# Kernel optimization log

Measured on AMD Instinct MI355X. Metric: run time of the kernel, lower is better.

Reference implementation:

```python
import jax, jax.numpy as jnp
import numpy as np

EPS = 1e-10
REG_WEIGHT = 1e-6  # regularization_weight passed to sparse_image_warp


def _phi(r):
    # TPS order-2 kernel on SQUARED distances r: 0.5 * r * log(r)
    return 0.5 * r * jnp.log(jnp.maximum(r, EPS))


def _sq_dist(a, b):
    # a: [b, n, 2], b: [b, m, 2] -> [b, n, m] squared euclidean distances
    aa = jnp.sum(a * a, axis=-1)[:, :, None]
    bb = jnp.sum(b * b, axis=-1)[:, None, :]
    ab = jnp.einsum('bnd,bmd->bnm', a, b)
    return jnp.maximum(aa + bb - 2.0 * ab, 0.0)


def interpolate_spline(train_points, train_values, query_points, reg_weight):
    # Solve polyharmonic (TPS, order 2) interpolation and evaluate at query points.
    b, n, _ = train_points.shape
    dt = train_points.dtype
    A = _phi(_sq_dist(train_points, train_points)) + reg_weight * jnp.eye(n, dtype=dt)
    B = jnp.concatenate([train_points, jnp.ones((b, n, 1), dt)], axis=-1)  # [b, n, 3]
    k = B.shape[-1]
    lhs = jnp.concatenate([
        jnp.concatenate([A, B], axis=-1),
        jnp.concatenate([jnp.swapaxes(B, 1, 2), jnp.zeros((b, k, k), dt)], axis=-1),
    ], axis=1)                                                             # [b, n+3, n+3]
    rhs = jnp.concatenate([train_values, jnp.zeros((b, k, train_values.shape[-1]), dt)], axis=1)
    sol = jnp.linalg.solve(lhs, rhs)
    w, v = sol[:, :n], sol[:, n:]                                          # [b,n,2], [b,3,2]
    Q = _phi(_sq_dist(query_points, train_points))                         # [b, m, n]
    qb = jnp.concatenate([query_points, jnp.ones((*query_points.shape[:2], 1), dt)], axis=-1)
    return Q @ w + qb @ v                                                  # [b, m, 2]


def dense_image_warp(image, flow):
    # image: [b, c, h, w] (NCHW), flow: [b, h, w, 2] in (y, x); sample at grid - flow.
    b, c, h, w = image.shape
    gy, gx = jnp.meshgrid(jnp.arange(h, dtype=flow.dtype),
                          jnp.arange(w, dtype=flow.dtype), indexing='ij')
    qy = jnp.clip(gy[None] - flow[..., 0], 0.0, h - 1.0)                  # [b, h, w]
    qx = jnp.clip(gx[None] - flow[..., 1], 0.0, w - 1.0)
    y0 = jnp.clip(jnp.floor(qy).astype(jnp.int32), 0, h - 2)
    x0 = jnp.clip(jnp.floor(qx).astype(jnp.int32), 0, w - 2)
    y1, x1 = y0 + 1, x0 + 1
    wy = (qy - y0.astype(flow.dtype))[..., None]                          # [b, h, w, 1]
    wx = (qx - x0.astype(flow.dtype))[..., None]
    bidx = jnp.arange(b)[:, None, None]

    def gather(yi, xi):
        # -> [b, h, w, c]
        return image[bidx, :, yi, xi]

    top = gather(y0, x0) * (1.0 - wx) + gather(y0, x1) * wx
    bot = gather(y1, x0) * (1.0 - wx) + gather(y1, x1) * wx
    out = top * (1.0 - wy) + bot * wy                                     # [b, h, w, c]
    return jnp.transpose(out, (0, 3, 1, 2))                               # back to NCHW


def sparse_image_warp(image, src_pts, dst_pts, reg_weight):
    # flows at control points, interpolated to a dense flow, then resample.
    b, _, h, w = image.shape
    flows = dst_pts - src_pts                                              # [b, n, 2]
    gy, gx = jnp.meshgrid(jnp.arange(h, dtype=src_pts.dtype),
                          jnp.arange(w, dtype=src_pts.dtype), indexing='ij')
    grid = jnp.stack([gy, gx], axis=-1).reshape(1, h * w, 2)
    query = jnp.broadcast_to(grid, (b, h * w, 2))
    dense_flow = interpolate_spline(dst_pts, flows, query, reg_weight).reshape(b, h, w, 2)
    return dense_image_warp(image, dense_flow), dense_flow


def setup_inputs() -> dict:
    key = jax.random.key(0)
    ks = jax.random.split(key, 10)
    B, C, H, W = 8, 3, 256, 256
    N_LDMARK = 68
    in_features = C * H * W

    def kaiming(k, fan_out, fan_in):
        bound = np.sqrt(6.0 / fan_in)
        return jax.random.uniform(k, (fan_out, fan_in), jnp.float32, -bound, bound)

    landmarks_mean = (jax.random.normal(ks[3], (N_LDMARK, 2), jnp.float32) * 50.0
                      + jnp.array([0.5 * H, 0.5 * W], jnp.float32)).reshape(-1)
    return {
        'x': jax.random.normal(ks[0], (B, C, H, W), jnp.float32),
        'images_rendered': jax.random.normal(ks[1], (B, 64, H, W), jnp.float32),
        'scales': jax.random.uniform(ks[2], (B, 1), jnp.float32),
        'landmarks_mean': landmarks_mean,
        'W1': kaiming(ks[4], 128, in_features),
        'b1': jnp.zeros((128,), jnp.float32),
        'W2': kaiming(ks[5], N_LDMARK * 2, 128),
        'b2': jnp.zeros((N_LDMARK * 2,), jnp.float32),
        'W3': kaiming(ks[6], N_LDMARK * 2, 128),
        'b3': jnp.zeros((N_LDMARK * 2,), jnp.float32),
    }


def reference(x, images_rendered, scales, landmarks_mean, W1, b1, W2, b2, W3, b3):
    b = x.shape[0]
    n_ldmark = W2.shape[0] // 2
    h = x.reshape(b, -1) @ W1.T + b1                                       # [b, 128]
    landmarks_pred = h @ W2.T + b2 + landmarks_mean                        # [b, 2n]
    landmarks_disp = (h @ W3.T + b3) * scales.reshape(-1, 1)               # [b, 2n]
    src = jax.lax.stop_gradient(landmarks_pred).reshape(b, n_ldmark, 2)
    dst = jax.lax.stop_gradient(landmarks_pred + landmarks_disp).reshape(b, n_ldmark, 2)
    landmarks_norm = jnp.mean(jnp.sqrt(jnp.sum(jnp.square(src - dst), axis=(1, 2))))
    warped, _ = sparse_image_warp(images_rendered, src, dst, REG_WEIGHT)
    return warped, landmarks_pred, landmarks_norm
```

## Files before the change

kernel.cpp:

```cpp
#include <hip/hip_runtime.h>
#include <math.h>

#define NB    8
#define CIMG  64
#define HH    256
#define WW    256
#define NL    68
#define NP    136
#define JD    128
#define NSYS  71
#define NCOL  73
#define MPAD  75
#define NCHK  32
#define CHUNK4 1536
#define ROW4  49152

#define OUT_PRED 33554432
#define OUT_NORM 33555520

#define WS_PART 0
#define WS_NORM 32768
#define WS_DST  32784
#define WS_WV   33920

__global__ __launch_bounds__(256) void k1_gemv(const float* __restrict__ x,
                                               const float* __restrict__ W1,
                                               float* __restrict__ part) {
  const int jg  = blockIdx.x;
  const int ch  = blockIdx.y;
  const int tid = threadIdx.x;
  const float4* __restrict__ xv = (const float4*)x;
  const float4* __restrict__ wv = (const float4*)W1;

  float acc[4][8];
#pragma unroll
  for (int a = 0; a < 4; ++a)
#pragma unroll
    for (int b = 0; b < 8; ++b) acc[a][b] = 0.f;

  const int base = ch * CHUNK4;
#pragma unroll
  for (int it = 0; it < 6; ++it) {
    const int k4 = base + it * 256 + tid;
    float4 w[4];
#pragma unroll
    for (int jj = 0; jj < 4; ++jj)
      w[jj] = wv[(size_t)(jg * 4 + jj) * ROW4 + k4];
#pragma unroll
    for (int b = 0; b < 8; ++b) {
      const float4 xr = xv[(size_t)b * ROW4 + k4];
#pragma unroll
      for (int jj = 0; jj < 4; ++jj) {
        acc[jj][b] = fmaf(w[jj].x, xr.x, acc[jj][b]);
        acc[jj][b] = fmaf(w[jj].y, xr.y, acc[jj][b]);
        acc[jj][b] = fmaf(w[jj].z, xr.z, acc[jj][b]);
        acc[jj][b] = fmaf(w[jj].w, xr.w, acc[jj][b]);
      }
    }
  }
#pragma unroll
  for (int jj = 0; jj < 4; ++jj)
#pragma unroll
    for (int b = 0; b < 8; ++b) {
      float v = acc[jj][b];
      for (int o = 32; o > 0; o >>= 1) v += __shfl_down(v, o, 64);
      acc[jj][b] = v;
    }
  __shared__ float sred[4][32];
  const int lane = tid & 63, wid = tid >> 6;
  if (lane == 0) {
#pragma unroll
    for (int jj = 0; jj < 4; ++jj)
#pragma unroll
      for (int b = 0; b < 8; ++b) sred[wid][jj * 8 + b] = acc[jj][b];
  }
  __syncthreads();
  if (tid < 32) {
    const float s = sred[0][tid] + sred[1][tid] + sred[2][tid] + sred[3][tid];
    const int jj = tid >> 3, b = tid & 7;
    part[((size_t)ch * JD + jg * 4 + jj) * 8 + b] = s;
  }
}

__device__ __forceinline__ double sys_entry(int r, int c,
                                            const float* s_dst,
                                            const float* s_disp) {
  if (r < NL) {
    if (c < NL) {
      const double dy = (double)s_dst[2 * r]     - (double)s_dst[2 * c];
      const double dx = (double)s_dst[2 * r + 1] - (double)s_dst[2 * c + 1];
      const double d2 = dy * dy + dx * dx;
      double v = 0.5 * d2 * log(fmax(d2, 1e-10));
      if (r == c) v += 1e-6;
      return v;
    }
    if (c == 68) return (double)s_dst[2 * r];
    if (c == 69) return (double)s_dst[2 * r + 1];
    if (c == 70) return 1.0;
    return (double)s_disp[2 * r + (c - 71)];
  }
  if (c < NL) {
    const int q = r - NL;
    return (q == 0) ? (double)s_dst[2 * c] : (q == 1) ? (double)s_dst[2 * c + 1] : 1.0;
  }
  return 0.0;
}

__global__ __launch_bounds__(256) void k2_land_solve(
    const float* __restrict__ part, const float* __restrict__ scales,
    const float* __restrict__ lmean, const float* __restrict__ b1,
    const float* __restrict__ W2, const float* __restrict__ b2,
    const float* __restrict__ W3, const float* __restrict__ b3,
    float* __restrict__ out, float* __restrict__ ws) {
  const int b = blockIdx.x, tid = threadIdx.x;
  const int lane = tid & 63, wv = tid >> 6;
  __shared__ float  s_h[JD];
  __shared__ float  s_dst[NP];
  __shared__ float  s_disp[NP];
  __shared__ double M[NSYS][MPAD];
  __shared__ int    s_perm[NSYS];
  __shared__ double s_inv;
  __shared__ int    s_pivv;

  if (tid < JD) {
    float s = b1[tid];
#pragma unroll 8
    for (int c = 0; c < NCHK; ++c) s += part[((size_t)c * JD + tid) * 8 + b];
    s_h[tid] = s;
  }
  __syncthreads();

  const float scale_b = scales[b];
  if (tid < NP) {
    const float4* w2 = (const float4*)(W2 + (size_t)tid * JD);
    const float4* w3 = (const float4*)(W3 + (size_t)tid * JD);
    float a2 = 0.f, a3 = 0.f;
#pragma unroll 8
    for (int k = 0; k < 32; ++k) {
      const float4 u = w2[k], v = w3[k];
      const float h0 = s_h[4 * k], h1 = s_h[4 * k + 1];
      const float h2 = s_h[4 * k + 2], h3 = s_h[4 * k + 3];
      a2 = fmaf(u.x, h0, fmaf(u.y, h1, fmaf(u.z, h2, fmaf(u.w, h3, a2))));
      a3 = fmaf(v.x, h0, fmaf(v.y, h1, fmaf(v.z, h2, fmaf(v.w, h3, a3))));
    }
    const float pred = a2 + b2[tid] + lmean[tid];
    const float disp = (a3 + b3[tid]) * scale_b;
    out[OUT_PRED + b * NP + tid] = pred;
    s_dst[tid]  = pred + disp;
    s_disp[tid] = disp;
  }
  __syncthreads();

  if (tid < 64) {
    float s = 0.f;
    for (int i = tid; i < NP; i += 64) { const float d = s_disp[i]; s = fmaf(d, d, s); }
    for (int o = 32; o > 0; o >>= 1) s += __shfl_down(s, o, 64);
    if (tid == 0) ws[WS_NORM + b] = s;
  }
  if (tid < NP) ws[WS_DST + b * NP + tid] = s_dst[tid];

  for (int e = tid; e < NSYS * NCOL; e += 256) {
    const int r = e / NCOL, c = e - r * NCOL;
    M[r][c] = sys_entry(r, c, s_dst, s_disp);
  }
  __syncthreads();

  const int rowA = lane, rowB = lane + 64;
  const bool hasB = (rowB < NSYS);
  bool actA = true, actB = hasB;
  int slotA = 0, slotB = 0;

#pragma unroll 1
  for (int p = 0; p < NSYS; ++p) {
    if (wv == 0) {
      unsigned ua = actA ? ((__float_as_uint((float)fabs(M[rowA][p])) & 0xFFFFFF80u) | (unsigned)rowA) : 0u;
      unsigned ub = (actB) ? ((__float_as_uint((float)fabs(M[rowB][p])) & 0xFFFFFF80u) | (unsigned)rowB) : 0u;
      unsigned u = ua > ub ? ua : ub;
#pragma unroll
      for (int o = 1; o < 64; o <<= 1) {
        const unsigned v = __shfl_xor(u, o);
        if (v > u) u = v;
      }
      const int piv = (int)(u & 0x7Fu);
      if (lane == 0) {
        s_pivv = piv;
        s_perm[p] = piv;
        s_inv = 1.0 / M[piv][p];
      }
    }
    __syncthreads();
    const int    piv = s_pivv;
    const double inv = s_inv;
    if (piv == rowA) { actA = false; slotA = p; }
    if (actB && piv == rowB) { actB = false; slotB = p; }
    const double mA = actA ? M[rowA][p] * inv : 0.0;
    const double mB = actB ? M[rowB][p] * inv : 0.0;

#pragma unroll 4
    for (int k = 0; k < 19; ++k) {
      const int c = wv + 4 * k;
      if (c > p && c < NCOL) {
        const double pvc = M[piv][c];
        if (actA) M[rowA][c] = fma(-mA, pvc, M[rowA][c]);
        if (actB) M[rowB][c] = fma(-mB, pvc, M[rowB][c]);
      }
    }
    __syncthreads();
  }

  if (wv == 0) {
    const int rpA = s_perm[lane];
    const int rpB = hasB ? s_perm[rowB] : 0;
    const double bb0a = M[rpA][NSYS], bb1a = M[rpA][NSYS + 1];
    const double diA = 1.0 / M[rpA][lane];
    double bb0b = 0.0, bb1b = 0.0, diB = 0.0;
    if (hasB) { bb0b = M[rpB][NSYS]; bb1b = M[rpB][NSYS + 1]; diB = 1.0 / M[rpB][rowB]; }
    double acc0a = 0.0, acc1a = 0.0, acc0b = 0.0, acc1b = 0.0;
    double sol0a = 0.0, sol1a = 0.0, sol0b = 0.0, sol1b = 0.0;
#pragma unroll 1
    for (int p = NSYS - 1; p >= 0; --p) {
      const double tA0 = (bb0a - acc0a) * diA;
      const double tA1 = (bb1a - acc1a) * diA;
      const double tB0 = (bb0b - acc0b) * diB;
      const double tB1 = (bb1b - acc1b) * diB;
      const bool fromB = (p >= 64);
      const int  src   = fromB ? (p - 64) : p;
      double x0 = fromB ? tB0 : tA0;
      double x1 = fromB ? tB1 : tA1;
      {
        const int lo0 = __builtin_amdgcn_readlane(__double2loint(x0), src);
        const int hi0 = __builtin_amdgcn_readlane(__double2hiint(x0), src);
        const int lo1 = __builtin_amdgcn_readlane(__double2loint(x1), src);
        const int hi1 = __builtin_amdgcn_readlane(__double2hiint(x1), src);
        x0 = __hiloint2double(hi0, lo0);
        x1 = __hiloint2double(hi1, lo1);
      }
      if (p >= 64) { if (lane == p - 64) { sol0b = tB0; sol1b = tB1; } }
      else         { if (lane == p)      { sol0a = tA0; sol1a = tA1; } }
      if (lane < p) {
        const double u2 = M[rpA][p];
        acc0a = fma(u2, x0, acc0a);
        acc1a = fma(u2, x1, acc1a);
      }
      if (hasB && rowB < p) {
        const double u2 = M[rpB][p];
        acc0b = fma(u2, x0, acc0b);
        acc1b = fma(u2, x1, acc1b);
      }
    }
    ws[WS_WV + (size_t)b * 142 + 2 * lane]     = (float)sol0a;
    ws[WS_WV + (size_t)b * 142 + 2 * lane + 1] = (float)sol1a;
    if (hasB) {
      ws[WS_WV + (size_t)b * 142 + 2 * rowB]     = (float)sol0b;
      ws[WS_WV + (size_t)b * 142 + 2 * rowB + 1] = (float)sol1b;
    }
  }
}

__global__ __launch_bounds__(256) void k3_warp(const float* __restrict__ img,
                                               const float* __restrict__ ws,
                                               float* __restrict__ out) {
  const int orig = blockIdx.x;
  const int wgid = (orig & 7) * 256 + (orig >> 3);
  const int b = wgid >> 8, y = wgid & 255;
  const int tid = threadIdx.x;

  if (orig == 0 && tid == 0) {
    float s = 0.f;
    for (int i = 0; i < NB; ++i) s += sqrtf(ws[WS_NORM + i]);
    out[OUT_NORM] = s * 0.125f;
  }

  __shared__ float s_c[NP], s_w[NP], s_v[6];
  if (tid < NP) {
    s_c[tid] = ws[WS_DST + b * NP + tid];
    s_w[tid] = ws[WS_WV + (size_t)b * 142 + tid];
  }
  if (tid >= NP && tid < NP + 6) s_v[tid - NP] = ws[WS_WV + (size_t)b * 142 + tid];
  __syncthreads();

  const float yf = (float)y, xf = (float)tid;
  float fy = fmaf(s_v[0], yf, fmaf(s_v[2], xf, s_v[4]));
  float fx = fmaf(s_v[1], yf, fmaf(s_v[3], xf, s_v[5]));
#pragma unroll 4
  for (int l = 0; l < NL; ++l) {
    const float dy = yf - s_c[2 * l];
    const float dx = xf - s_c[2 * l + 1];
    const float r  = fmaf(dy, dy, dx * dx);
    const float ph = 0.5f * r * __logf(fmaxf(r, 1e-10f));
    fy = fmaf(s_w[2 * l],     ph, fy);
    fx = fmaf(s_w[2 * l + 1], ph, fx);
  }

  const float qy = fminf(fmaxf(yf - fy, 0.f), 255.f);
  const float qx = fminf(fmaxf(xf - fx, 0.f), 255.f);
  int y0 = (int)floorf(qy); y0 = y0 > 254 ? 254 : y0;
  int x0 = (int)floorf(qx); x0 = x0 > 254 ? 254 : x0;
  const float wy = qy - (float)y0, wx = qx - (float)x0;
  const float w00 = (1.f - wy) * (1.f - wx), w01 = (1.f - wy) * wx;
  const float w10 = wy * (1.f - wx),         w11 = wy * wx;

  const float* p0 = img + (size_t)b * CIMG * 65536 + y0 * 256 + x0;
  const size_t ob = (size_t)b * CIMG * 65536 + (size_t)y * 256 + tid;
#pragma unroll 4
  for (int c = 0; c < CIMG; ++c) {
    const float* p = p0 + (size_t)c * 65536;
    const float v00 = p[0], v01 = p[1], v10 = p[256], v11 = p[257];
    const float val = fmaf(w00, v00, fmaf(w01, v01, fmaf(w10, v10, w11 * v11)));
    __builtin_nontemporal_store(val, &out[ob + (size_t)c * 65536]);
  }
}

extern "C" void kernel_launch(void* const* d_in, const int* in_sizes, int n_in,
                              void* d_out, int out_size, void* d_ws, size_t ws_size,
                              hipStream_t stream) {
  const float* x      = (const float*)d_in[0];
  const float* img    = (const float*)d_in[1];
  const float* scales = (const float*)d_in[2];
  const float* lmean  = (const float*)d_in[3];
  const float* W1     = (const float*)d_in[4];
  const float* b1     = (const float*)d_in[5];
  const float* W2     = (const float*)d_in[6];
  const float* b2     = (const float*)d_in[7];
  const float* W3     = (const float*)d_in[8];
  const float* b3     = (const float*)d_in[9];
  float* out = (float*)d_out;
  float* ws  = (float*)d_ws;

  k1_gemv<<<dim3(32, 32), 256, 0, stream>>>(x, W1, ws + WS_PART);
  k2_land_solve<<<NB, 256, 0, stream>>>(ws + WS_PART, scales, lmean, b1, W2, b2, W3, b3, out, ws);
  k3_warp<<<NB * HH, 256, 0, stream>>>(img, ws, out);
}
```

Before: 249.0 us.

## Fuse pivot search into row-parallel elimination with one barrier per step

Restructures the in-shared-memory LU elimination in k2_land_solve. Rows are now split across the four waves and columns across lanes, and each active row is updated along its full width. While updating, each wave computes its best candidate for the next pivot, so the separate single-wave pivot search and the second barrier per step go away. Only four per-wave candidates are reduced at the start of each step. The cost is some redundant updating of already-eliminated columns, and the single barrier leaves a possible race on the candidate slots in shared memory.

```diff
diff --git a/kernel.cpp b/kernel.cpp
--- a/kernel.cpp
+++ b/kernel.cpp
@@ -23,6 +23,12 @@
 #define WS_DST  32784
 #define WS_WV   33920
 
+__device__ __forceinline__ double rl_f64(double v, int sl) {
+  const int lo = __builtin_amdgcn_readlane(__double2loint(v), sl);
+  const int hi = __builtin_amdgcn_readlane(__double2hiint(v), sl);
+  return __hiloint2double(hi, lo);
+}
+
 __global__ __launch_bounds__(256) void k1_gemv(const float* __restrict__ x,
                                                const float* __restrict__ W1,
                                                float* __restrict__ part) {
@@ -119,8 +125,8 @@
   __shared__ float  s_disp[NP];
   __shared__ double M[NSYS][MPAD];
   __shared__ int    s_perm[NSYS];
-  __shared__ double s_inv;
-  __shared__ int    s_pivv;
+  __shared__ double s_cand_v[4];
+  __shared__ unsigned s_cand_p[4];
 
   if (tid < JD) {
     float s = b1[tid];
@@ -165,50 +171,74 @@
   }
   __syncthreads();
 
-  const int rowA = lane, rowB = lane + 64;
-  const bool hasB = (rowB < NSYS);
-  bool actA = true, actB = hasB;
-  int slotA = 0, slotB = 0;
+  unsigned long long actLo = ~0ull;
+  unsigned actHi = 0x7Fu;
+  {
+    unsigned bpk = 0u; double bval = 0.0;
+#pragma unroll 1
+    for (int k = 0; k < 18; ++k) {
+      const int r = wv + 4 * k;
+      if (r < NSYS) {
+        const double v = M[r][0];
+        const unsigned pk = (__float_as_uint((float)fabs(v)) & 0xFFFFFF80u) | (unsigned)r;
+        if (pk > bpk) { bpk = pk; bval = v; }
+      }
+    }
+    if (lane == 0) { s_cand_p[wv] = bpk; s_cand_v[wv] = bval; }
+  }
 
 #pragma unroll 1
   for (int p = 0; p < NSYS; ++p) {
-    if (wv == 0) {
-      unsigned ua = actA ? ((__float_as_uint((float)fabs(M[rowA][p])) & 0xFFFFFF80u) | (unsigned)rowA) : 0u;
-      unsigned ub = (actB) ? ((__float_as_uint((float)fabs(M[rowB][p])) & 0xFFFFFF80u) | (unsigned)rowB) : 0u;
-      unsigned u = ua > ub ? ua : ub;
-#pragma unroll
-      for (int o = 1; o < 64; o <<= 1) {
-        const unsigned v = __shfl_xor(u, o);
-        if (v > u) u = v;
-      }
-      const int piv = (int)(u & 0x7Fu);
-      if (lane == 0) {
-        s_pivv = piv;
-        s_perm[p] = piv;
-        s_inv = 1.0 / M[piv][p];
-      }
-    }
     __syncthreads();
-    const int    piv = s_pivv;
-    const double inv = s_inv;
-    if (piv == rowA) { actA = false; slotA = p; }
-    if (actB && piv == rowB) { actB = false; slotB = p; }
-    const double mA = actA ? M[rowA][p] * inv : 0.0;
-    const double mB = actB ? M[rowB][p] * inv : 0.0;
-
-#pragma unroll 4
-    for (int k = 0; k < 19; ++k) {
-      const int c = wv + 4 * k;
-      if (c > p && c < NCOL) {
-        const double pvc = M[piv][c];
-        if (actA) M[rowA][c] = fma(-mA, pvc, M[rowA][c]);
-        if (actB) M[rowB][c] = fma(-mB, pvc, M[rowB][c]);
-      }
-    }
-    __syncthreads();
-  }
+    unsigned bpk = s_cand_p[0]; double bval = s_cand_v[0];
+    {
+      const unsigned pk1 = s_cand_p[1]; const double v1 = s_cand_v[1];
+      if (pk1 > bpk) { bpk = pk1; bval = v1; }
+      const unsigned pk2 = s_cand_p[2]; const double v2 = s_cand_v[2];
+      if (pk2 > bpk) { bpk = pk2; bval = v2; }
+      const unsigned pk3 = s_cand_p[3]; const double v3 = s_cand_v[3];
+      if (pk3 > bpk) { bpk = pk3; bval = v3; }
+    }
+    const int    piv = (int)(bpk & 0x7Fu);
+    const double inv = 1.0 / bval;
+    if (tid == 0) s_perm[p] = piv;
+    if (piv < 64) actLo &= ~(1ull << piv); else actHi &= ~(1u << (piv - 64));
+
+    const double u0 = M[piv][lane];
+    const double u1 = (lane < 9) ? M[piv][lane + 64] : 0.0;
+
+    const int pn = p + 1;
+    unsigned nbpk = 0u; double nbval = 0.0;
+#pragma unroll 1
+    for (int k = 0; k < 18; ++k) {
+      const int r = wv + 4 * k;
+      if (r < NSYS) {
+        const bool act = (r < 64) ? (((actLo >> r) & 1ull) != 0)
+                                  : (((actHi >> (r - 64)) & 1u) != 0);
+        if (act) {
+          const double m  = M[r][p] * inv;
+          const double v0 = M[r][lane];
+          const double n0 = fma(-m, u0, v0);
+          M[r][lane] = n0;
+          double n1 = 0.0;
+          if (lane < 9) {
+            const double v1 = M[r][lane + 64];
+            n1 = fma(-m, u1, v1);
+            M[r][lane + 64] = n1;
+          }
+          const double cnew = (pn < 64) ? rl_f64(n0, pn) : rl_f64(n1, pn - 64);
+          const unsigned pk = (__float_as_uint((float)fabs(cnew)) & 0xFFFFFF80u) | (unsigned)r;
+          if (pk > nbpk) { nbpk = pk; nbval = cnew; }
+        }
+      }
+    }
+    if (lane == 0) { s_cand_p[wv] = nbpk; s_cand_v[wv] = nbval; }
+  }
+  __syncthreads();
 
   if (wv == 0) {
+    const int rowB = lane + 64;
+    const bool hasB = (rowB < NSYS);
     const int rpA = s_perm[lane];
     const int rpB = hasB ? s_perm[rowB] : 0;
     const double bb0a = M[rpA][NSYS], bb1a = M[rpA][NSYS + 1];
@@ -227,14 +257,8 @@
       const int  src   = fromB ? (p - 64) : p;
       double x0 = fromB ? tB0 : tA0;
       double x1 = fromB ? tB1 : tA1;
-      {
-        const int lo0 = __builtin_amdgcn_readlane(__double2loint(x0), src);
-        const int hi0 = __builtin_amdgcn_readlane(__double2hiint(x0), src);
-        const int lo1 = __builtin_amdgcn_readlane(__double2loint(x1), src);
-        const int hi1 = __builtin_amdgcn_readlane(__double2hiint(x1), src);
-        x0 = __hiloint2double(hi0, lo0);
-        x1 = __hiloint2double(hi1, lo1);
-      }
+      x0 = rl_f64(x0, src);
+      x1 = rl_f64(x1, src);
       if (p >= 64) { if (lane == p - 64) { sol0b = tB0; sol1b = tB1; } }
       else         { if (lane == p)      { sol0a = tA0; sol1a = tA1; } }
       if (lane < p) {
```

Result: slower. 346.7 us (+39.2%).

## Solve spline system in fp32 registers with fp64 iterative refinement on a single wavefront

Applied to the files above, without the earlier changes.

The landmark solve kernel drops to one 64-lane wavefront. It runs the Gaussian elimination in fp32 with each lane holding two full matrix rows in registers, and broadcasts pivot rows through readlane, so there are no block-wide barriers or LDS traffic per pivot step. The L multipliers and U factors are saved to shared memory, and two rounds of fp64 residual-based iterative refinement restore accuracy. This removes the per-pivot __syncthreads and fp64 LDS updates of the serial solve. In exchange it adds refinement passes, high register pressure from the 146-float row arrays, and a risk of reduced accuracy if the fp32 factorization is poorly conditioned.

```diff
diff --git a/kernel.cpp b/kernel.cpp
--- a/kernel.cpp
+++ b/kernel.cpp
@@ -10,7 +10,7 @@
 #define JD    128
 #define NSYS  71
 #define NCOL  73
-#define MPAD  75
+#define M64P  75
 #define NCHK  32
 #define CHUNK4 1536
 #define ROW4  49152
@@ -22,6 +22,15 @@
 #define WS_NORM 32768
 #define WS_DST  32784
 #define WS_WV   33920
+
+__device__ __forceinline__ double rl_f64(double v, int sl) {
+  const int lo = __builtin_amdgcn_readlane(__double2loint(v), sl);
+  const int hi = __builtin_amdgcn_readlane(__double2hiint(v), sl);
+  return __hiloint2double(hi, lo);
+}
+__device__ __forceinline__ float rl_f32(float v, int sl) {
+  return __int_as_float(__builtin_amdgcn_readlane(__float_as_int(v), sl));
+}
 
 __global__ __launch_bounds__(256) void k1_gemv(const float* __restrict__ x,
                                                const float* __restrict__ W1,
@@ -106,34 +115,34 @@
   return 0.0;
 }
 
-__global__ __launch_bounds__(256) void k2_land_solve(
+__global__ __launch_bounds__(64, 1) void k2_land_solve(
     const float* __restrict__ part, const float* __restrict__ scales,
     const float* __restrict__ lmean, const float* __restrict__ b1,
     const float* __restrict__ W2, const float* __restrict__ b2,
     const float* __restrict__ W3, const float* __restrict__ b3,
     float* __restrict__ out, float* __restrict__ ws) {
-  const int b = blockIdx.x, tid = threadIdx.x;
-  const int lane = tid & 63, wv = tid >> 6;
+  const int b = blockIdx.x, lane = threadIdx.x;
   __shared__ float  s_h[JD];
   __shared__ float  s_dst[NP];
   __shared__ float  s_disp[NP];
-  __shared__ double M[NSYS][MPAD];
+  __shared__ double M64[NSYS][M64P];
+  __shared__ float  Ud[NCOL][72];
+  __shared__ float  Lm[NSYS][72];
+  __shared__ double yds0[NSYS], yds1[NSYS];
   __shared__ int    s_perm[NSYS];
-  __shared__ double s_inv;
-  __shared__ int    s_pivv;
-
-  if (tid < JD) {
-    float s = b1[tid];
+
+  for (int j = lane; j < JD; j += 64) {
+    float s = b1[j];
 #pragma unroll 8
-    for (int c = 0; c < NCHK; ++c) s += part[((size_t)c * JD + tid) * 8 + b];
-    s_h[tid] = s;
+    for (int c = 0; c < NCHK; ++c) s += part[((size_t)c * JD + j) * 8 + b];
+    s_h[j] = s;
   }
   __syncthreads();
 
   const float scale_b = scales[b];
-  if (tid < NP) {
-    const float4* w2 = (const float4*)(W2 + (size_t)tid * JD);
-    const float4* w3 = (const float4*)(W3 + (size_t)tid * JD);
+  for (int i = lane; i < NP; i += 64) {
+    const float4* w2 = (const float4*)(W2 + (size_t)i * JD);
+    const float4* w3 = (const float4*)(W3 + (size_t)i * JD);
     float a2 = 0.f, a3 = 0.f;
 #pragma unroll 8
     for (int k = 0; k < 32; ++k) {
@@ -143,117 +152,204 @@
       a2 = fmaf(u.x, h0, fmaf(u.y, h1, fmaf(u.z, h2, fmaf(u.w, h3, a2))));
       a3 = fmaf(v.x, h0, fmaf(v.y, h1, fmaf(v.z, h2, fmaf(v.w, h3, a3))));
     }
-    const float pred = a2 + b2[tid] + lmean[tid];
-    const float disp = (a3 + b3[tid]) * scale_b;
-    out[OUT_PRED + b * NP + tid] = pred;
-    s_dst[tid]  = pred + disp;
-    s_disp[tid] = disp;
+    const float pred = a2 + b2[i] + lmean[i];
+    const float disp = (a3 + b3[i]) * scale_b;
+    out[OUT_PRED + b * NP + i] = pred;
+    s_dst[i]  = pred + disp;
+    s_disp[i] = disp;
   }
   __syncthreads();
 
-  if (tid < 64) {
+  {
     float s = 0.f;
-    for (int i = tid; i < NP; i += 64) { const float d = s_disp[i]; s = fmaf(d, d, s); }
+    for (int i = lane; i < NP; i += 64) {
+      const float d = s_disp[i];
+      s = fmaf(d, d, s);
+      ws[WS_DST + b * NP + i] = s_dst[i];
+    }
     for (int o = 32; o > 0; o >>= 1) s += __shfl_down(s, o, 64);
-    if (tid == 0) ws[WS_NORM + b] = s;
-  }
-  if (tid < NP) ws[WS_DST + b * NP + tid] = s_dst[tid];
-
-  for (int e = tid; e < NSYS * NCOL; e += 256) {
-    const int r = e / NCOL, c = e - r * NCOL;
-    M[r][c] = sys_entry(r, c, s_dst, s_disp);
-  }
-  __syncthreads();
+    if (lane == 0) ws[WS_NORM + b] = s;
+  }
 
   const int rowA = lane, rowB = lane + 64;
   const bool hasB = (rowB < NSYS);
+  float fA[NCOL], fB[NCOL];
+#pragma unroll
+  for (int c = 0; c < NCOL; ++c) {
+    const double eA = sys_entry(rowA, c, s_dst, s_disp);
+    M64[rowA][c] = eA;
+    fA[c] = (float)eA;
+    double eB = 0.0;
+    if (hasB) { eB = sys_entry(rowB, c, s_dst, s_disp); M64[rowB][c] = eB; }
+    fB[c] = (float)eB;
+  }
+
+  float cvA = fA[0], cvB = fB[0];
   bool actA = true, actB = hasB;
   int slotA = 0, slotB = 0;
-
 #pragma unroll 1
   for (int p = 0; p < NSYS; ++p) {
-    if (wv == 0) {
-      unsigned ua = actA ? ((__float_as_uint((float)fabs(M[rowA][p])) & 0xFFFFFF80u) | (unsigned)rowA) : 0u;
-      unsigned ub = (actB) ? ((__float_as_uint((float)fabs(M[rowB][p])) & 0xFFFFFF80u) | (unsigned)rowB) : 0u;
-      unsigned u = ua > ub ? ua : ub;
-#pragma unroll
-      for (int o = 1; o < 64; o <<= 1) {
-        const unsigned v = __shfl_xor(u, o);
-        if (v > u) u = v;
-      }
-      const int piv = (int)(u & 0x7Fu);
-      if (lane == 0) {
-        s_pivv = piv;
-        s_perm[p] = piv;
-        s_inv = 1.0 / M[piv][p];
-      }
-    }
-    __syncthreads();
-    const int    piv = s_pivv;
-    const double inv = s_inv;
+    unsigned ua = actA ? ((__float_as_uint(fabsf(cvA)) & 0xFFFFFF80u) | (unsigned)rowA) : 0u;
+    unsigned ub = actB ? ((__float_as_uint(fabsf(cvB)) & 0xFFFFFF80u) | (unsigned)rowB) : 0u;
+    unsigned u = ua > ub ? ua : ub;
+#pragma unroll
+    for (int o = 1; o < 64; o <<= 1) {
+      const unsigned v = __shfl_xor(u, o);
+      if (v > u) u = v;
+    }
+    const int piv = __builtin_amdgcn_readfirstlane((int)(u & 0x7Fu));
+    const bool pB = piv >= 64;
+    const int  pl = pB ? piv - 64 : piv;
+    const float pvA = rl_f32(cvA, pl), pvB = rl_f32(cvB, pl);
+    const float inv = 1.0f / (pB ? pvB : pvA);
     if (piv == rowA) { actA = false; slotA = p; }
     if (actB && piv == rowB) { actB = false; slotB = p; }
-    const double mA = actA ? M[rowA][p] * inv : 0.0;
-    const double mB = actB ? M[rowB][p] * inv : 0.0;
-
-#pragma unroll 4
-    for (int k = 0; k < 19; ++k) {
-      const int c = wv + 4 * k;
-      if (c > p && c < NCOL) {
-        const double pvc = M[piv][c];
-        if (actA) M[rowA][c] = fma(-mA, pvc, M[rowA][c]);
-        if (actB) M[rowB][c] = fma(-mB, pvc, M[rowB][c]);
+    const float mA = actA ? cvA * inv : 0.0f;
+    const float mB = actB ? cvB * inv : 0.0f;
+    Lm[p][lane] = mA;
+    if (lane < 7) Lm[p][64 + lane] = mB;
+    if (lane == 0) s_perm[p] = piv;
+
+    if (pB) {
+#pragma unroll
+      for (int g = 0; g < 10; ++g) {
+        if (g * 8 + 7 > p) {
+#pragma unroll
+          for (int cc = 0; cc < 8; ++cc) {
+            const int c = g * 8 + cc;
+            if (c < NCOL) {
+              const float pr = rl_f32(fB[c], pl);
+              fA[c] = fmaf(-mA, pr, fA[c]);
+              fB[c] = fmaf(-mB, pr, fB[c]);
+            }
+          }
+        }
       }
-    }
+    } else {
+#pragma unroll
+      for (int g = 0; g < 10; ++g) {
+        if (g * 8 + 7 > p) {
+#pragma unroll
+          for (int cc = 0; cc < 8; ++cc) {
+            const int c = g * 8 + cc;
+            if (c < NCOL) {
+              const float pr = rl_f32(fA[c], pl);
+              fA[c] = fmaf(-mA, pr, fA[c]);
+              fB[c] = fmaf(-mB, pr, fB[c]);
+            }
+          }
+        }
+      }
+    }
+    const int pn = p + 1;
+#pragma unroll
+    for (int g = 0; g < 10; ++g) {
+      if (pn >= g * 8 && pn < g * 8 + 8) {
+#pragma unroll
+        for (int cc = 0; cc < 8; ++cc) {
+          const int c = g * 8 + cc;
+          if (c < NCOL && c == pn) { cvA = fA[c]; cvB = fB[c]; }
+        }
+      }
+    }
+  }
+
+#pragma unroll
+  for (int c = 0; c < NCOL; ++c) {
+    Ud[c][slotA] = fA[c];
+    if (hasB) Ud[c][slotB] = fB[c];
+  }
+  __syncthreads();
+
+  double sol0a, sol1a, sol0b = 0.0, sol1b = 0.0;
+  const double diA = 1.0 / (double)Ud[lane][lane];
+  const double diB = hasB ? 1.0 / (double)Ud[rowB][rowB] : 1.0;
+#define BACKSUB(BB0A, BB1A, BB0B, BB1B, O0A, O1A, O0B, O1B)                     \
+  {                                                                             \
+    double bb0a = (BB0A), bb1a = (BB1A), bb0b = (BB0B), bb1b = (BB1B);          \
+    double acc0a = 0.0, acc1a = 0.0, acc0b = 0.0, acc1b = 0.0;                  \
+    double s0a = 0.0, s1a = 0.0, s0b = 0.0, s1b = 0.0;                          \
+    _Pragma("unroll 1")                                                         \
+    for (int p = NSYS - 1; p >= 0; --p) {                                       \
+      const double tA0 = (bb0a - acc0a) * diA;                                  \
+      const double tA1 = (bb1a - acc1a) * diA;                                  \
+      const double tB0 = (bb0b - acc0b) * diB;                                  \
+      const double tB1 = (bb1b - acc1b) * diB;                                  \
+      const bool fromB = (p >= 64);                                             \
+      const int  src   = fromB ? (p - 64) : p;                                  \
+      const double x0 = rl_f64(fromB ? tB0 : tA0, src);                         \
+      const double x1 = rl_f64(fromB ? tB1 : tA1, src);                         \
+      if (p >= 64) { if (lane == p - 64) { s0b = tB0; s1b = tB1; } }            \
+      else         { if (lane == p)      { s0a = tA0; s1a = tA1; } }            \
+      if (lane < p) {                                                           \
+        const double u2 = (double)Ud[p][lane];                                  \
+        acc0a = fma(u2, x0, acc0a);                                             \
+        acc1a = fma(u2, x1, acc1a);                                             \
+      }                                                                         \
+      if (hasB && rowB < p) {                                                   \
+        const double u2 = (double)Ud[p][rowB];                                  \
+        acc0b = fma(u2, x0, acc0b);                                             \
+        acc1b = fma(u2, x1, acc1b);                                             \
+      }                                                                         \
+    }                                                                           \
+    O0A = s0a; O1A = s1a; O0B = s0b; O1B = s1b;                                 \
+  }
+
+  BACKSUB((double)Ud[NSYS][lane], (double)Ud[NSYS + 1][lane],
+          hasB ? (double)Ud[NSYS][rowB] : 0.0, hasB ? (double)Ud[NSYS + 1][rowB] : 0.0,
+          sol0a, sol1a, sol0b, sol1b)
+
+#pragma unroll 1
+  for (int it = 0; it < 2; ++it) {
+    double r0A = M64[rowA][71], r1A = M64[rowA][72];
+    double r0B = hasB ? M64[rowB][71] : 0.0;
+    double r1B = hasB ? M64[rowB][72] : 0.0;
+#pragma unroll 1
+    for (int c = 0; c < 64; ++c) {
+      const double x0 = rl_f64(sol0a, c), x1 = rl_f64(sol1a, c);
+      const double a = M64[rowA][c];
+      r0A = fma(-a, x0, r0A); r1A = fma(-a, x1, r1A);
+      const double bm = hasB ? M64[rowB][c] : 0.0;
+      r0B = fma(-bm, x0, r0B); r1B = fma(-bm, x1, r1B);
+    }
+#pragma unroll 1
+    for (int c = 64; c < NSYS; ++c) {
+      const double x0 = rl_f64(sol0b, c - 64), x1 = rl_f64(sol1b, c - 64);
+      const double a = M64[rowA][c];
+      r0A = fma(-a, x0, r0A); r1A = fma(-a, x1, r1A);
+      const double bm = hasB ? M64[rowB][c] : 0.0;
+      r0B = fma(-bm, x0, r0B); r1B = fma(-bm, x1, r1B);
+    }
+#pragma unroll 1
+    for (int p = 0; p < NSYS; ++p) {
+      const int pvv = __builtin_amdgcn_readfirstlane(s_perm[p]);
+      const bool pB2 = pvv >= 64;
+      const int  pl2 = pB2 ? pvv - 64 : pvv;
+      const double yp0 = pB2 ? rl_f64(r0B, pl2) : rl_f64(r0A, pl2);
+      const double yp1 = pB2 ? rl_f64(r1B, pl2) : rl_f64(r1A, pl2);
+      const double lA = (double)Lm[p][lane];
+      r0A = fma(-lA, yp0, r0A); r1A = fma(-lA, yp1, r1A);
+      const double lB = (lane < 7) ? (double)Lm[p][64 + lane] : 0.0;
+      r0B = fma(-lB, yp0, r0B); r1B = fma(-lB, yp1, r1B);
+    }
+    yds0[rowA] = r0A; yds1[rowA] = r1A;
+    if (hasB) { yds0[rowB] = r0B; yds1[rowB] = r1B; }
     __syncthreads();
-  }
-
-  if (wv == 0) {
-    const int rpA = s_perm[lane];
-    const int rpB = hasB ? s_perm[rowB] : 0;
-    const double bb0a = M[rpA][NSYS], bb1a = M[rpA][NSYS + 1];
-    const double diA = 1.0 / M[rpA][lane];
-    double bb0b = 0.0, bb1b = 0.0, diB = 0.0;
-    if (hasB) { bb0b = M[rpB][NSYS]; bb1b = M[rpB][NSYS + 1]; diB = 1.0 / M[rpB][rowB]; }
-    double acc0a = 0.0, acc1a = 0.0, acc0b = 0.0, acc1b = 0.0;
-    double sol0a = 0.0, sol1a = 0.0, sol0b = 0.0, sol1b = 0.0;
-#pragma unroll 1
-    for (int p = NSYS - 1; p >= 0; --p) {
-      const double tA0 = (bb0a - acc0a) * diA;
-      const double tA1 = (bb1a - acc1a) * diA;
-      const double tB0 = (bb0b - acc0b) * diB;
-      const double tB1 = (bb1b - acc1b) * diB;
-      const bool fromB = (p >= 64);
-      const int  src   = fromB ? (p - 64) : p;
-      double x0 = fromB ? tB0 : tA0;
-      double x1 = fromB ? tB1 : tA1;
-      {
-        const int lo0 = __builtin_amdgcn_readlane(__double2loint(x0), src);
-        const int hi0 = __builtin_amdgcn_readlane(__double2hiint(x0), src);
-        const int lo1 = __builtin_amdgcn_readlane(__double2loint(x1), src);
-        const int hi1 = __builtin_amdgcn_readlane(__double2hiint(x1), src);
-        x0 = __hiloint2double(hi0, lo0);
-        x1 = __hiloint2double(hi1, lo1);
-      }
-      if (p >= 64) { if (lane == p - 64) { sol0b = tB0; sol1b = tB1; } }
-      else         { if (lane == p)      { sol0a = tA0; sol1a = tA1; } }
-      if (lane < p) {
-        const double u2 = M[rpA][p];
-        acc0a = fma(u2, x0, acc0a);
-        acc1a = fma(u2, x1, acc1a);
-      }
-      if (hasB && rowB < p) {
-        const double u2 = M[rpB][p];
-        acc0b = fma(u2, x0, acc0b);
-        acc1b = fma(u2, x1, acc1b);
-      }
-    }
-    ws[WS_WV + (size_t)b * 142 + 2 * lane]     = (float)sol0a;
-    ws[WS_WV + (size_t)b * 142 + 2 * lane + 1] = (float)sol1a;
-    if (hasB) {
-      ws[WS_WV + (size_t)b * 142 + 2 * rowB]     = (float)sol0b;
-      ws[WS_WV + (size_t)b * 142 + 2 * rowB + 1] = (float)sol1b;
-    }
+    const int prA = s_perm[lane];
+    const int prB = hasB ? s_perm[rowB] : 0;
+    double d0a, d1a, d0b, d1b;
+    BACKSUB(yds0[prA], yds1[prA],
+            hasB ? yds0[prB] : 0.0, hasB ? yds1[prB] : 0.0,
+            d0a, d1a, d0b, d1b)
+    sol0a += d0a; sol1a += d1a; sol0b += d0b; sol1b += d1b;
+    __syncthreads();
+  }
+
+  ws[WS_WV + (size_t)b * 142 + 2 * rowA]     = (float)sol0a;
+  ws[WS_WV + (size_t)b * 142 + 2 * rowA + 1] = (float)sol1a;
+  if (hasB) {
+    ws[WS_WV + (size_t)b * 142 + 2 * rowB]     = (float)sol0b;
+    ws[WS_WV + (size_t)b * 142 + 2 * rowB + 1] = (float)sol1b;
   }
 }
 
@@ -328,6 +424,6 @@
   float* ws  = (float*)d_ws;
 
   k1_gemv<<<dim3(32, 32), 256, 0, stream>>>(x, W1, ws + WS_PART);
-  k2_land_solve<<<NB, 256, 0, stream>>>(ws + WS_PART, scales, lmean, b1, W2, b2, W3, b3, out, ws);
+  k2_land_solve<<<NB, 64, 0, stream>>>(ws + WS_PART, scales, lmean, b1, W2, b2, W3, b3, out, ws);
   k3_warp<<<NB * HH, 256, 0, stream>>>(img, ws, out);
 }
```

Result: slower. 378.0 us (+51.8%).
